# Kernel optimization log

Hardware: AMD Instinct MI355X
Metric: run time of the kernel (lower is better)

The kernel has to match this reference:

```python
import jax, jax.numpy as jnp
import numpy as np

NPOINT = 2048
NSAMPLE = 16
LEAKY = 0.1
BN_EPS = 1e-5


def square_distance(src, dst):
    # src [B,S,3], dst [B,N,3] -> [B,S,N] squared euclidean
    d = -2.0 * jnp.einsum('bsc,bnc->bsn', src, dst)
    d = d + jnp.sum(src * src, -1)[:, :, None]
    d = d + jnp.sum(dst * dst, -1)[:, None, :]
    return d


def furthest_point_sample(xyz, npoint):
    # xyz [B,N,3] -> idx [B,npoint]; matches pointnet2 CUDA (seed = index 0)
    B, N, _ = xyz.shape

    def step(carry, _):
        dist, far = carry  # dist [B,N], far [B]
        centroid = jnp.take_along_axis(xyz, far[:, None, None], axis=1)  # [B,1,3]
        d = jnp.sum((xyz - centroid) ** 2, axis=-1)
        dist = jnp.minimum(dist, d)
        nxt = jnp.argmax(dist, axis=-1).astype(jnp.int32)
        return (dist, nxt), far

    init = (jnp.full((B, N), 1e10, xyz.dtype), jnp.zeros((B,), jnp.int32))
    _, idxs = jax.lax.scan(step, init, None, length=npoint)
    return idxs.T  # [B, npoint]


def _gather_nbrs(p, i):
    # p [N,C], i [S,K] -> [S,K,C]
    return p[i]


gather_group = jax.vmap(_gather_nbrs)


def conv_bn_lrelu(x, W, g, b):
    # x [B,Cin,S,K], W [Cout,Cin]; 1x1 conv + train-mode BatchNorm2d + LeakyReLU
    y = jnp.einsum('oc,bcsk->bosk', W, x)
    mean = jnp.mean(y, axis=(0, 2, 3), keepdims=True)
    var = jnp.var(y, axis=(0, 2, 3), keepdims=True)
    y = (y - mean) * jax.lax.rsqrt(var + BN_EPS)
    y = y * g[None, :, None, None] + b[None, :, None, None]
    return jnp.where(y > 0, y, LEAKY * y)


def setup_inputs() -> dict:
    key = jax.random.key(0)
    ks = jax.random.split(key, 5)
    B, N, D = 4, 8192, 64
    return {
        'xyz': jax.random.normal(ks[0], (B, 3, N), jnp.float32),
        'points': jax.random.normal(ks[1], (B, D, N), jnp.float32),
        'conv0_w': jax.random.normal(ks[2], (64, 67), jnp.float32) * 0.05,
        'conv1_w': jax.random.normal(ks[3], (64, 64), jnp.float32) * 0.05,
        'conv2_w': jax.random.normal(ks[4], (128, 64), jnp.float32) * 0.05,
        'bn0_g': jnp.ones((64,), jnp.float32),
        'bn0_b': jnp.zeros((64,), jnp.float32),
        'bn1_g': jnp.ones((64,), jnp.float32),
        'bn1_b': jnp.zeros((64,), jnp.float32),
        'bn2_g': jnp.ones((128,), jnp.float32),
        'bn2_b': jnp.zeros((128,), jnp.float32),
    }


def reference(xyz, points, conv0_w, conv1_w, conv2_w,
              bn0_g, bn0_b, bn1_g, bn1_b, bn2_g, bn2_b):
    xyz_t = jnp.transpose(xyz, (0, 2, 1))      # [B,N,3]
    pts_t = jnp.transpose(points, (0, 2, 1))   # [B,N,D]

    fps_idx = furthest_point_sample(xyz_t, NPOINT)                       # [B,S]
    new_xyz = jnp.take_along_axis(xyz_t, fps_idx[:, :, None], axis=1)    # [B,S,3]

    sqrd = square_distance(new_xyz, xyz_t)                               # [B,S,N]
    _, idx = jax.lax.top_k(-sqrd, NSAMPLE)                               # [B,S,K]

    grouped_xyz = gather_group(xyz_t, idx)                               # [B,S,K,3]
    grouped_norm = grouped_xyz - new_xyz[:, :, None, :]
    grouped_pts = gather_group(pts_t, idx)                               # [B,S,K,D]
    new_points = jnp.concatenate([grouped_norm, grouped_pts], axis=-1)   # [B,S,K,D+3]
    new_points = jnp.transpose(new_points, (0, 3, 1, 2))                 # [B,D+3,S,K]

    for W, g, b in ((conv0_w, bn0_g, bn0_b), (conv1_w, bn1_g, bn1_b),
                    (conv2_w, bn2_g, bn2_b)):
        new_points = conv_bn_lrelu(new_points, W, g, b)

    feat = jnp.max(new_points, axis=-1)                                  # [B,128,S]
    return jnp.transpose(new_xyz, (0, 2, 1)), feat, fps_idx
```

## Files before the change

### kernel.cpp

```cpp
#include <hip/hip_runtime.h>
#include <hip/hip_bf16.h>

#define BB 4
#define NP 8192
#define SS 2048
#define KK 16
#define DD 64
#define NN (BB*SS*KK)
#define HEATERS 128

typedef float vf2 __attribute__((ext_vector_type(2)));

#if defined(__has_builtin)
#if __has_builtin(__builtin_amdgcn_permlane16_swap) && __has_builtin(__builtin_amdgcn_permlane32_swap)
#define HAVE_PERMLANE_SWAP 1
#endif
#endif

__device__ __forceinline__ float wave_max_f32(float v) {
  int x;
  x = __builtin_amdgcn_update_dpp(0, __float_as_int(v), 0xB1, 0xF, 0xF, true);
  v = fmaxf(v, __int_as_float(x));
  x = __builtin_amdgcn_update_dpp(0, __float_as_int(v), 0x4E, 0xF, 0xF, true);
  v = fmaxf(v, __int_as_float(x));
  x = __builtin_amdgcn_update_dpp(0, __float_as_int(v), 0x141, 0xF, 0xF, true);
  v = fmaxf(v, __int_as_float(x));
  x = __builtin_amdgcn_update_dpp(0, __float_as_int(v), 0x140, 0xF, 0xF, true);
  v = fmaxf(v, __int_as_float(x));
#ifdef HAVE_PERMLANE_SWAP
  {
    unsigned u = __float_as_uint(v);
    auto r16 = __builtin_amdgcn_permlane16_swap(u, u, false, false);
    v = fmaxf(__uint_as_float(r16[0]), __uint_as_float(r16[1]));
    unsigned u2 = __float_as_uint(v);
    auto r32 = __builtin_amdgcn_permlane32_swap(u2, u2, false, false);
    v = fmaxf(__uint_as_float(r32[0]), __uint_as_float(r32[1]));
  }
#else
  x = __builtin_amdgcn_ds_swizzle(__float_as_int(v), 0x401F);
  v = fmaxf(v, __int_as_float(x));
  v = fmaxf(v, __shfl_xor(v, 32, 64));
#endif
  return v;
}

__global__ __launch_bounds__(512) void fps_kernel(
    const float* __restrict__ xyz, float* __restrict__ newXyz,
    float* __restrict__ out, int* __restrict__ done)
{
  const int t = threadIdx.x;
  int* prog = done + 16;

  if (blockIdx.x >= BB) {
    float a0 = 1.0f, a1 = 1.1f, a2 = 1.2f, a3 = 1.3f;
    const float bm = 1.000001f, cm = 1e-7f;
    bool hot = false;
    for (;;) {
      if (!hot) {
        for (int k = 0; k < 1024; k++) {
          a0 = __builtin_fmaf(a0, bm, cm);
          a1 = __builtin_fmaf(a1, bm, cm);
          a2 = __builtin_fmaf(a2, bm, cm);
          a3 = __builtin_fmaf(a3, bm, cm);
        }
        if (__hip_atomic_load(done, __ATOMIC_RELAXED, __HIP_MEMORY_SCOPE_AGENT) >= BB)
          break;
        if (__hip_atomic_load(prog, __ATOMIC_RELAXED, __HIP_MEMORY_SCOPE_AGENT) >= 1792)
          hot = true;
      } else {
        vf2 p0 = {a0, 1.5f}, p1 = {a1, 1.6f}, p2 = {a2, 1.7f}, p3 = {a3, 1.8f};
        const vf2 pb = {1.000001f, 0.999999f};
        const vf2 pc = {1e-7f, 1e-7f};
        for (;;) {
          for (int k = 0; k < 256; k++) {
            p0 = p0 * pb + pc; p1 = p1 * pb + pc;
            p2 = p2 * pb + pc; p3 = p3 * pb + pc;
          }
          if (__hip_atomic_load(done, __ATOMIC_RELAXED, __HIP_MEMORY_SCOPE_AGENT) >= BB)
            break;
        }
        a0 = p0.x + p0.y; a1 = p1.x + p1.y; a2 = p2.x + p2.y; a3 = p3.x + p3.y;
        break;
      }
    }
    if (a0 == 123.456f && a1 == 2.f && a2 == 3.f && a3 == 4.f)
      ((volatile int*)done)[1] = 1;
    return;
  }

  const int b = blockIdx.x;
  const float* xb = xyz + (size_t)b * 3 * NP;

  __shared__ float lx[NP], ly[NP], lz[NP];
  __shared__ int   wis[SS];
  __shared__ unsigned long long swin[3];

  vf2 px[8], py[8], pz[8], dist[8];
  const int i0 = t << 4;
#pragma unroll
  for (int h = 0; h < 8; h++) {
    int i = i0 + (h << 1);
    vf2 x = *(const vf2*)(xb + i);
    vf2 y = *(const vf2*)(xb + NP + i);
    vf2 z = *(const vf2*)(xb + 2 * NP + i);
    px[h] = x; py[h] = y; pz[h] = z;
    dist[h] = (vf2){1e10f, 1e10f};
    *(vf2*)(lx + i) = x; *(vf2*)(ly + i) = y; *(vf2*)(lz + i) = z;
  }
  if (t == 0) { wis[0] = 0; swin[0] = 0; swin[1] = 0; swin[2] = 0; }
  __syncthreads();

  float cx = lx[0], cy = ly[0], cz = lz[0];

  for (int it = 1; it < SS; ++it) {
    vf2 c2x = {cx, cx}, c2y = {cy, cy}, c2z = {cz, cz};
    vf2 lb = {-1.0f, -1.0f};
    {
#pragma clang fp contract(off)
#pragma unroll
      for (int h = 0; h < 8; h++) {
        vf2 dx = px[h] - c2x;
        vf2 dy = py[h] - c2y;
        vf2 dz = pz[h] - c2z;
        vf2 d  = (dx * dx + dy * dy) + dz * dz;
        vf2 dm = __builtin_elementwise_min(dist[h], d);
        dist[h] = dm;
        lb = __builtin_elementwise_max(lb, dm);
      }
    }
    float lbest = fmaxf(lb.x, lb.y);
    float Vw = wave_max_f32(lbest);
    int q = it % 3;
    if (lbest == Vw) {
      unsigned mi = 0u;
#pragma unroll
      for (int h = 7; h >= 0; h--) {
        unsigned base = (unsigned)(i0 + (h << 1));
        if (dist[h].y == Vw) mi = base + 1;
        if (dist[h].x == Vw) mi = base;
      }
      unsigned long long pk =
          ((unsigned long long)__float_as_uint(Vw) << 32) | (unsigned)(~mi);
      atomicMax(&swin[q], pk);
    }
    __syncthreads();
    unsigned long long pkf = swin[q];
    int ii = (int)(~((unsigned)pkf));
    if (t == 0) {
      wis[it] = ii; swin[(q + 2) % 3] = 0;
      if ((it & 255) == 0)
        __hip_atomic_store(prog, it, __ATOMIC_RELAXED, __HIP_MEMORY_SCOPE_AGENT);
    }
    cx = lx[ii]; cy = ly[ii]; cz = lz[ii];
  }
  __syncthreads();

  float* outX = out;
  float* outI = out + 24576 + 1048576;
  for (int s = t; s < SS; s += 512) {
    int iw = wis[s];
    float x = lx[iw], y = ly[iw], z = lz[iw];
    size_t qq = (size_t)(b * SS + s);
    newXyz[qq * 3 + 0] = x;
    newXyz[qq * 3 + 1] = y;
    newXyz[qq * 3 + 2] = z;
    outX[(b * 3 + 0) * SS + s] = x;
    outX[(b * 3 + 1) * SS + s] = y;
    outX[(b * 3 + 2) * SS + s] = z;
    outI[b * SS + s] = (float)iw;
  }
  if (t == 0)
    __hip_atomic_fetch_add(done, 1, __ATOMIC_RELEASE, __HIP_MEMORY_SCOPE_AGENT);
}

__global__ __launch_bounds__(256) void knn_kernel(
    const float* __restrict__ xyz, const float* __restrict__ newXyz,
    int* __restrict__ knnIdx)
{
  const int t = threadIdx.x, w = t >> 6, l = t & 63;
  const int q = blockIdx.x * 4 + w;
  const int b = q >> 11;
  const float* xb = xyz + (size_t)b * 3 * NP;
  float qx = newXyz[q * 3], qy = newXyz[q * 3 + 1], qz = newXyz[q * 3 + 2];
  float ss = __fadd_rn(__fadd_rn(__fmul_rn(qx, qx), __fmul_rn(qy, qy)), __fmul_rn(qz, qz));
  float kd[16]; int ki[16];
#pragma unroll
  for (int j = 0; j < 16; j++) { kd[j] = __builtin_inff(); ki[j] = 0x7fffffff; }

  for (int m = 0; m < 32; m++) {
    int i = (m << 8) + (l << 2);
    float4 xv = *(const float4*)(xb + i);
    float4 yv = *(const float4*)(xb + NP + i);
    float4 zv = *(const float4*)(xb + 2 * NP + i);
#pragma unroll
    for (int c = 0; c < 4; c++) {
      float x = (c == 0) ? xv.x : (c == 1) ? xv.y : (c == 2) ? xv.z : xv.w;
      float y = (c == 0) ? yv.x : (c == 1) ? yv.y : (c == 2) ? yv.z : yv.w;
      float z = (c == 0) ? zv.x : (c == 1) ? zv.y : (c == 2) ? zv.z : zv.w;
      float dot = __fadd_rn(__fadd_rn(__fmul_rn(x, qx), __fmul_rn(y, qy)), __fmul_rn(z, qz));
      float nn  = __fadd_rn(__fadd_rn(__fmul_rn(x, x), __fmul_rn(y, y)), __fmul_rn(z, z));
      float d   = __fadd_rn(__fadd_rn(__fmul_rn(-2.0f, dot), ss), nn);
      if (d < kd[15]) {
        kd[15] = d; ki[15] = i + c;
#pragma unroll
        for (int jj = 15; jj >= 1; jj--) {
          if (kd[jj] < kd[jj - 1]) {
            float td = kd[jj]; kd[jj] = kd[jj - 1]; kd[jj - 1] = td;
            int   ti = ki[jj]; ki[jj] = ki[jj - 1]; ki[jj - 1] = ti;
          }
        }
      }
    }
  }

  __shared__ float sd[4 * 64 * 17];
  __shared__ int   sx[4 * 64 * 17];
  int base = (w * 64 + l) * 17;
#pragma unroll
  for (int j = 0; j < 16; j++) { sd[base + j] = kd[j]; sx[base + j] = ki[j]; }
  __syncthreads();

  int cur = 0; int outIdx = 0;
#pragma unroll 1
  for (int r = 0; r < 16; r++) {
    float hv = (cur < 16) ? sd[base + cur] : __builtin_inff();
    int   hi = (cur < 16) ? sx[base + cur] : 0x7fffffff;
    int   hl = l;
#pragma unroll
    for (int m2 = 1; m2 < 64; m2 <<= 1) {
      float ov = __shfl_xor(hv, m2, 64);
      int   oi = __shfl_xor(hi, m2, 64);
      int   ol = __shfl_xor(hl, m2, 64);
      if (ov < hv || (ov == hv && oi < hi)) { hv = ov; hi = oi; hl = ol; }
    }
    if (l == hl) cur++;
    if (l == r) outIdx = hi;
  }
  if (l < 16) knnIdx[q * 16 + l] = outIdx;
}

__global__ __launch_bounds__(256) void conv0_kernel(
    const float* __restrict__ xyz, const float* __restrict__ points,
    const float* __restrict__ newXyz, const int* __restrict__ knnIdx,
    const float* __restrict__ W, float* __restrict__ Y)
{
  int n = blockIdx.x * 256 + threadIdx.x;
  int b = n >> 15;
  int q = n >> 4;
  int ip = knnIdx[n];
  const float* xb = xyz + (size_t)b * 3 * NP;
  float x[67];
  x[0] = xb[ip]          - newXyz[q * 3 + 0];
  x[1] = xb[NP + ip]     - newXyz[q * 3 + 1];
  x[2] = xb[2 * NP + ip] - newXyz[q * 3 + 2];
  const float* pb = points + (size_t)b * DD * NP + ip;
#pragma unroll 8
  for (int d0 = 0; d0 < DD; d0++)
    x[3 + d0] = pb[(size_t)d0 * NP];
#pragma unroll 1
  for (int o = 0; o < 64; o += 4) {
    float a0 = 0.f, a1 = 0.f, a2 = 0.f, a3 = 0.f;
#pragma unroll
    for (int c = 0; c < 67; c++) {
      float xv = x[c];
      a0 = fmaf(W[(o + 0) * 67 + c], xv, a0);
      a1 = fmaf(W[(o + 1) * 67 + c], xv, a1);
      a2 = fmaf(W[(o + 2) * 67 + c], xv, a2);
      a3 = fmaf(W[(o + 3) * 67 + c], xv, a3);
    }
    Y[(size_t)(o + 0) * NN + n] = a0;
    Y[(size_t)(o + 1) * NN + n] = a1;
    Y[(size_t)(o + 2) * NN + n] = a2;
    Y[(size_t)(o + 3) * NN + n] = a3;
  }
}

template <int CIN, int COUT>
__global__ __launch_bounds__(256) void conv_bn_kernel(
    const float* __restrict__ X, const float* __restrict__ W,
    const float* __restrict__ stats, const float* __restrict__ g,
    const float* __restrict__ bt, float* __restrict__ Y)
{
  __shared__ vf2 sss[CIN];
  if (threadIdx.x < CIN) {
    int c = threadIdx.x;
    float mean = stats[c * 2] * (1.0f / NN);
    float var  = stats[c * 2 + 1] * (1.0f / NN) - mean * mean;
    float inv  = rsqrtf(var + 1e-5f);
    float sc = inv * g[c];
    float sh = bt[c] - mean * sc;
    sss[c] = (vf2){sc, sh};
  }
  __syncthreads();
  int n = blockIdx.x * 256 + threadIdx.x;
  float x[CIN];
#pragma unroll
  for (int c = 0; c < CIN; c++) x[c] = X[(size_t)c * NN + n];
#pragma unroll
  for (int c = 0; c < CIN; c++) {
    vf2 p = sss[c];
    float v = fmaf(x[c], p.x, p.y);
    x[c] = v > 0.0f ? v : 0.1f * v;
  }
#pragma unroll 1
  for (int o = 0; o < COUT; o += 4) {
    float a0 = 0.f, a1 = 0.f, a2 = 0.f, a3 = 0.f;
#pragma unroll
    for (int c = 0; c < CIN; c++) {
      float xv = x[c];
      a0 = fmaf(W[(o + 0) * CIN + c], xv, a0);
      a1 = fmaf(W[(o + 1) * CIN + c], xv, a1);
      a2 = fmaf(W[(o + 2) * CIN + c], xv, a2);
      a3 = fmaf(W[(o + 3) * CIN + c], xv, a3);
    }
    Y[(size_t)(o + 0) * NN + n] = a0;
    Y[(size_t)(o + 1) * NN + n] = a1;
    Y[(size_t)(o + 2) * NN + n] = a2;
    Y[(size_t)(o + 3) * NN + n] = a3;
  }
}

__global__ __launch_bounds__(256) void stats_kernel(
    const float* __restrict__ Y, float* __restrict__ stats)
{
  int c = blockIdx.y;
  int base = blockIdx.x * 4096 + threadIdx.x;
  const float* yc = Y + (size_t)c * NN;
  float s1 = 0.f, s2 = 0.f;
#pragma unroll
  for (int j = 0; j < 16; j++) {
    float v = yc[base + j * 256];
    s1 += v; s2 = fmaf(v, v, s2);
  }
#pragma unroll
  for (int m = 1; m < 64; m <<= 1) {
    s1 += __shfl_xor(s1, m, 64);
    s2 += __shfl_xor(s2, m, 64);
  }
  __shared__ float r1[4], r2[4];
  int w = threadIdx.x >> 6;
  if ((threadIdx.x & 63) == 0) { r1[w] = s1; r2[w] = s2; }
  __syncthreads();
  if (threadIdx.x == 0) {
    float t1 = r1[0] + r1[1] + r1[2] + r1[3];
    float t2 = r2[0] + r2[1] + r2[2] + r2[3];
    atomicAdd(&stats[c * 2], t1);
    atomicAdd(&stats[c * 2 + 1], t2);
  }
}

__global__ __launch_bounds__(256) void maxk_kernel(
    const float* __restrict__ X, const float* __restrict__ stats,
    const float* __restrict__ g, const float* __restrict__ bt,
    float* __restrict__ out)
{
  int m = blockIdx.x * 256 + threadIdx.x;
  int s = m & 2047;
  int o = (m >> 11) & 127;
  int b = m >> 18;
  float mean = stats[o * 2] * (1.0f / NN);
  float var  = stats[o * 2 + 1] * (1.0f / NN) - mean * mean;
  float inv  = rsqrtf(var + 1e-5f);
  float sc = inv * g[o];
  float sh = bt[o] - mean * sc;
  const float4* p = (const float4*)(X + (size_t)o * NN + ((size_t)((b << 11) + s) << 4));
  float mx = -__builtin_inff();
#pragma unroll
  for (int j = 0; j < 4; j++) {
    float4 v4 = p[j];
    float a = fmaf(v4.x, sc, sh); a = a > 0.f ? a : 0.1f * a;
    float b2 = fmaf(v4.y, sc, sh); b2 = b2 > 0.f ? b2 : 0.1f * b2;
    float c = fmaf(v4.z, sc, sh); c = c > 0.f ? c : 0.1f * c;
    float d = fmaf(v4.w, sc, sh); d = d > 0.f ? d : 0.1f * d;
    mx = fmaxf(mx, fmaxf(fmaxf(a, b2), fmaxf(c, d)));
  }
  out[24576 + (size_t)((b << 7) + o) * SS + s] = mx;
}

extern "C" void kernel_launch(void* const* d_in, const int* in_sizes, int n_in,
                              void* d_out, int out_size, void* d_ws, size_t ws_size,
                              hipStream_t stream) {
  const float* xyz    = (const float*)d_in[0];
  const float* points = (const float*)d_in[1];
  const float* w0 = (const float*)d_in[2];
  const float* w1 = (const float*)d_in[3];
  const float* w2 = (const float*)d_in[4];
  const float* g0 = (const float*)d_in[5];
  const float* b0 = (const float*)d_in[6];
  const float* g1 = (const float*)d_in[7];
  const float* b1 = (const float*)d_in[8];
  const float* g2 = (const float*)d_in[9];
  const float* b2 = (const float*)d_in[10];
  float* out = (float*)d_out;

  float* wsf    = (float*)d_ws;
  float* newXyz = wsf;
  int*   knnIdx = (int*)(wsf + 24576);
  float* stats0 = wsf + 155648;
  float* stats1 = wsf + 155904;
  float* stats2 = wsf + 156160;
  int*   done   = (int*)(wsf + 157440);
  float* Xa     = wsf + 160000;
  float* Xb     = wsf + 8941824;

  hipMemsetAsync(stats0, 0, 2048 * 4, stream);

  fps_kernel<<<BB + HEATERS, 512, 0, stream>>>(xyz, newXyz, out, done);
  knn_kernel<<<SS * BB / 4, 256, 0, stream>>>(xyz, newXyz, knnIdx);

  conv0_kernel<<<NN / 256, 256, 0, stream>>>(xyz, points, newXyz, knnIdx, w0, Xb);
  stats_kernel<<<dim3(32, 64), 256, 0, stream>>>(Xb, stats0);

  conv_bn_kernel<64, 64><<<NN / 256, 256, 0, stream>>>(Xb, w1, stats0, g0, b0, Xa);
  stats_kernel<<<dim3(32, 64), 256, 0, stream>>>(Xa, stats1);

  conv_bn_kernel<64, 128><<<NN / 256, 256, 0, stream>>>(Xa, w2, stats1, g1, b1, Xb);
  stats_kernel<<<dim3(32, 128), 256, 0, stream>>>(Xb, stats2);

  maxk_kernel<<<(BB * 128 * SS) / 256, 256, 0, stream>>>(Xb, stats2, g2, b2, out);
}
```

Before: 2.251 ms.

## Fuse kNN search into FPS kernel using the spinning heater blocks as workers

Removes the separate kNN kernel and has the extra blocks launched alongside the four FPS blocks wait until FPS completes, then run the kNN top-16 search in a grid-stride loop over queries. The idle-wait loop is reworked with s_sleep and a short unrolled FMA burst instead of a long FMA loop. The aim is to drop a kernel launch and its tail, and to have worker blocks already resident when FPS finishes. Each worker block now reserves the large FPS shared-memory footprint, which limits occupancy for the kNN phase. Only four of the eight waves per block do kNN work, and correctness depends on the acquire load seeing newXyz.

```diff
diff --git a/kernel.cpp b/kernel.cpp
--- a/kernel.cpp
+++ b/kernel.cpp
@@ -7,7 +7,7 @@
 #define KK 16
 #define DD 64
 #define NN (BB*SS*KK)
-#define HEATERS 128
+#define WORKERS 251
 
 typedef float vf2 __attribute__((ext_vector_type(2)));
 
@@ -46,54 +46,118 @@
 
 __global__ __launch_bounds__(512) void fps_kernel(
     const float* __restrict__ xyz, float* __restrict__ newXyz,
-    float* __restrict__ out, int* __restrict__ done)
+    float* __restrict__ out, int* __restrict__ done, int* __restrict__ knnIdx)
 {
   const int t = threadIdx.x;
   int* prog = done + 16;
 
+  __shared__ float lx[NP], ly[NP], lz[NP];
+  __shared__ int   wis[SS];
+  __shared__ unsigned long long swin[3];
+  __shared__ float wsd[4 * 64 * 17];
+  __shared__ int   wsx[4 * 64 * 17];
+
   if (blockIdx.x >= BB) {
-    float a0 = 1.0f, a1 = 1.1f, a2 = 1.2f, a3 = 1.3f;
-    const float bm = 1.000001f, cm = 1e-7f;
-    bool hot = false;
-    for (;;) {
-      if (!hot) {
-        for (int k = 0; k < 1024; k++) {
-          a0 = __builtin_fmaf(a0, bm, cm);
-          a1 = __builtin_fmaf(a1, bm, cm);
-          a2 = __builtin_fmaf(a2, bm, cm);
-          a3 = __builtin_fmaf(a3, bm, cm);
-        }
+    const int w = t >> 6, l = t & 63;
+    float hacc = 0.0f;
+    {
+      float h0 = 1.0f, h1 = 1.1f, h2 = 1.2f, h3 = 1.3f;
+      vf2 p0 = {1.0f, 1.5f}, p1 = {1.1f, 1.6f}, p2 = {1.2f, 1.7f}, p3 = {1.3f, 1.8f};
+      const vf2 pb = {1.000001f, 0.999999f};
+      const vf2 pc = {1e-7f, 1e-7f};
+      bool hot = false;
+      for (;;) {
         if (__hip_atomic_load(done, __ATOMIC_RELAXED, __HIP_MEMORY_SCOPE_AGENT) >= BB)
           break;
-        if (__hip_atomic_load(prog, __ATOMIC_RELAXED, __HIP_MEMORY_SCOPE_AGENT) >= 1792)
-          hot = true;
-      } else {
-        vf2 p0 = {a0, 1.5f}, p1 = {a1, 1.6f}, p2 = {a2, 1.7f}, p3 = {a3, 1.8f};
-        const vf2 pb = {1.000001f, 0.999999f};
-        const vf2 pc = {1e-7f, 1e-7f};
-        for (;;) {
+        if (!hot) {
+#pragma unroll
+          for (int k = 0; k < 64; k++) {
+            h0 = __builtin_fmaf(h0, 1.000001f, 1e-7f);
+            h1 = __builtin_fmaf(h1, 1.000001f, 1e-7f);
+            h2 = __builtin_fmaf(h2, 1.000001f, 1e-7f);
+            h3 = __builtin_fmaf(h3, 1.000001f, 1e-7f);
+          }
+          __builtin_amdgcn_s_sleep(64);
+          if (__hip_atomic_load(prog, __ATOMIC_RELAXED, __HIP_MEMORY_SCOPE_AGENT) >= 1792)
+            hot = true;
+        } else {
           for (int k = 0; k < 256; k++) {
             p0 = p0 * pb + pc; p1 = p1 * pb + pc;
             p2 = p2 * pb + pc; p3 = p3 * pb + pc;
           }
-          if (__hip_atomic_load(done, __ATOMIC_RELAXED, __HIP_MEMORY_SCOPE_AGENT) >= BB)
-            break;
         }
-        a0 = p0.x + p0.y; a1 = p1.x + p1.y; a2 = p2.x + p2.y; a3 = p3.x + p3.y;
-        break;
       }
-    }
-    if (a0 == 123.456f && a1 == 2.f && a2 == 3.f && a3 == 4.f)
+      hacc += h0 + h1 + h2 + h3 + p0.x + p1.x + p2.x + p3.x + p0.y + p1.y + p2.y + p3.y;
+    }
+    if (hacc == 123.456f)
       ((volatile int*)done)[1] = 1;
+    (void)__hip_atomic_load(done, __ATOMIC_ACQUIRE, __HIP_MEMORY_SCOPE_AGENT);
+    if (w >= 4) return;
+
+    const int base = (w * 64 + l) * 17;
+    for (unsigned q = (blockIdx.x - BB) * 4 + (unsigned)w; q < (unsigned)(BB * SS);
+         q += WORKERS * 4) {
+      const int b = q >> 11;
+      const float* xb = xyz + (size_t)b * 3 * NP;
+      const float* nx = newXyz + (size_t)q * 3;
+      float qx = nx[0], qy = nx[1], qz = nx[2];
+      float ssq = __fadd_rn(__fadd_rn(__fmul_rn(qx, qx), __fmul_rn(qy, qy)), __fmul_rn(qz, qz));
+      float kd[16]; int ki[16];
+#pragma unroll
+      for (int j = 0; j < 16; j++) { kd[j] = __builtin_inff(); ki[j] = 0x7fffffff; }
+
+      for (int m = 0; m < 32; m++) {
+        int i = (m << 8) + (l << 2);
+        float4 xv = *(const float4*)(xb + i);
+        float4 yv = *(const float4*)(xb + NP + i);
+        float4 zv = *(const float4*)(xb + 2 * NP + i);
+#pragma unroll
+        for (int c = 0; c < 4; c++) {
+          float x = (c == 0) ? xv.x : (c == 1) ? xv.y : (c == 2) ? xv.z : xv.w;
+          float y = (c == 0) ? yv.x : (c == 1) ? yv.y : (c == 2) ? yv.z : yv.w;
+          float z = (c == 0) ? zv.x : (c == 1) ? zv.y : (c == 2) ? zv.z : zv.w;
+          float dot = __fadd_rn(__fadd_rn(__fmul_rn(x, qx), __fmul_rn(y, qy)), __fmul_rn(z, qz));
+          float nn  = __fadd_rn(__fadd_rn(__fmul_rn(x, x), __fmul_rn(y, y)), __fmul_rn(z, z));
+          float d   = __fadd_rn(__fadd_rn(__fmul_rn(-2.0f, dot), ssq), nn);
+          if (d < kd[15]) {
+            kd[15] = d; ki[15] = i + c;
+#pragma unroll
+            for (int jj = 15; jj >= 1; jj--) {
+              if (kd[jj] < kd[jj - 1]) {
+                float td = kd[jj]; kd[jj] = kd[jj - 1]; kd[jj - 1] = td;
+                int   ti = ki[jj]; ki[jj] = ki[jj - 1]; ki[jj - 1] = ti;
+              }
+            }
+          }
+        }
+      }
+
+#pragma unroll
+      for (int j = 0; j < 16; j++) { wsd[base + j] = kd[j]; wsx[base + j] = ki[j]; }
+
+      int cur = 0; int outIdx = 0;
+#pragma unroll 1
+      for (int r = 0; r < 16; r++) {
+        float hv = (cur < 16) ? wsd[base + cur] : __builtin_inff();
+        int   hi = (cur < 16) ? wsx[base + cur] : 0x7fffffff;
+        int   hl = l;
+#pragma unroll
+        for (int m2 = 1; m2 < 64; m2 <<= 1) {
+          float ov = __shfl_xor(hv, m2, 64);
+          int   oi = __shfl_xor(hi, m2, 64);
+          int   ol = __shfl_xor(hl, m2, 64);
+          if (ov < hv || (ov == hv && oi < hi)) { hv = ov; hi = oi; hl = ol; }
+        }
+        if (l == hl) cur++;
+        if (l == r) outIdx = hi;
+      }
+      if (l < 16) knnIdx[q * 16 + l] = outIdx;
+    }
     return;
   }
 
   const int b = blockIdx.x;
   const float* xb = xyz + (size_t)b * 3 * NP;
-
-  __shared__ float lx[NP], ly[NP], lz[NP];
-  __shared__ int   wis[SS];
-  __shared__ unsigned long long swin[3];
 
   vf2 px[8], py[8], pz[8], dist[8];
   const int i0 = t << 4;
@@ -171,72 +235,6 @@
   }
   if (t == 0)
     __hip_atomic_fetch_add(done, 1, __ATOMIC_RELEASE, __HIP_MEMORY_SCOPE_AGENT);
-}
-
-__global__ __launch_bounds__(256) void knn_kernel(
-    const float* __restrict__ xyz, const float* __restrict__ newXyz,
-    int* __restrict__ knnIdx)
-{
-  const int t = threadIdx.x, w = t >> 6, l = t & 63;
-  const int q = blockIdx.x * 4 + w;
-  const int b = q >> 11;
-  const float* xb = xyz + (size_t)b * 3 * NP;
-  float qx = newXyz[q * 3], qy = newXyz[q * 3 + 1], qz = newXyz[q * 3 + 2];
-  float ss = __fadd_rn(__fadd_rn(__fmul_rn(qx, qx), __fmul_rn(qy, qy)), __fmul_rn(qz, qz));
-  float kd[16]; int ki[16];
-#pragma unroll
-  for (int j = 0; j < 16; j++) { kd[j] = __builtin_inff(); ki[j] = 0x7fffffff; }
-
-  for (int m = 0; m < 32; m++) {
-    int i = (m << 8) + (l << 2);
-    float4 xv = *(const float4*)(xb + i);
-    float4 yv = *(const float4*)(xb + NP + i);
-    float4 zv = *(const float4*)(xb + 2 * NP + i);
-#pragma unroll
-    for (int c = 0; c < 4; c++) {
-      float x = (c == 0) ? xv.x : (c == 1) ? xv.y : (c == 2) ? xv.z : xv.w;
-      float y = (c == 0) ? yv.x : (c == 1) ? yv.y : (c == 2) ? yv.z : yv.w;
-      float z = (c == 0) ? zv.x : (c == 1) ? zv.y : (c == 2) ? zv.z : zv.w;
-      float dot = __fadd_rn(__fadd_rn(__fmul_rn(x, qx), __fmul_rn(y, qy)), __fmul_rn(z, qz));
-      float nn  = __fadd_rn(__fadd_rn(__fmul_rn(x, x), __fmul_rn(y, y)), __fmul_rn(z, z));
-      float d   = __fadd_rn(__fadd_rn(__fmul_rn(-2.0f, dot), ss), nn);
-      if (d < kd[15]) {
-        kd[15] = d; ki[15] = i + c;
-#pragma unroll
-        for (int jj = 15; jj >= 1; jj--) {
-          if (kd[jj] < kd[jj - 1]) {
-            float td = kd[jj]; kd[jj] = kd[jj - 1]; kd[jj - 1] = td;
-            int   ti = ki[jj]; ki[jj] = ki[jj - 1]; ki[jj - 1] = ti;
-          }
-        }
-      }
-    }
-  }
-
-  __shared__ float sd[4 * 64 * 17];
-  __shared__ int   sx[4 * 64 * 17];
-  int base = (w * 64 + l) * 17;
-#pragma unroll
-  for (int j = 0; j < 16; j++) { sd[base + j] = kd[j]; sx[base + j] = ki[j]; }
-  __syncthreads();
-
-  int cur = 0; int outIdx = 0;
-#pragma unroll 1
-  for (int r = 0; r < 16; r++) {
-    float hv = (cur < 16) ? sd[base + cur] : __builtin_inff();
-    int   hi = (cur < 16) ? sx[base + cur] : 0x7fffffff;
-    int   hl = l;
-#pragma unroll
-    for (int m2 = 1; m2 < 64; m2 <<= 1) {
-      float ov = __shfl_xor(hv, m2, 64);
-      int   oi = __shfl_xor(hi, m2, 64);
-      int   ol = __shfl_xor(hl, m2, 64);
-      if (ov < hv || (ov == hv && oi < hi)) { hv = ov; hi = oi; hl = ol; }
-    }
-    if (l == hl) cur++;
-    if (l == r) outIdx = hi;
-  }
-  if (l < 16) knnIdx[q * 16 + l] = outIdx;
 }
 
 __global__ __launch_bounds__(256) void conv0_kernel(
@@ -405,8 +403,7 @@
 
   hipMemsetAsync(stats0, 0, 2048 * 4, stream);
 
-  fps_kernel<<<BB + HEATERS, 512, 0, stream>>>(xyz, newXyz, out, done);
-  knn_kernel<<<SS * BB / 4, 256, 0, stream>>>(xyz, newXyz, knnIdx);
+  fps_kernel<<<BB + WORKERS, 512, 0, stream>>>(xyz, newXyz, out, done, knnIdx);
 
   conv0_kernel<<<NN / 256, 256, 0, stream>>>(xyz, points, newXyz, knnIdx, w0, Xb);
   stats_kernel<<<dim3(32, 64), 256, 0, stream>>>(Xb, stats0);
```

After: 2.699 ms. +19.9%, slower.
